# Kernel optimization log

Hardware: AMD Instinct MI355X
Metric: run time of the kernel (lower is better)

## Reference

```python
import jax, jax.numpy as jnp
import numpy as np

B, H, W, C = 8, 128, 128, 256
L = H * W
PROJ = max(C // 2, 128)
LN_EPS = 1e-5
MAX_DIST = 1.414


def _grid_edges(h, w):
    # 4-connected grid edges (bidirectional), shape (E, 2), E = 4hw - 2(h+w)
    idx = np.arange(h * w, dtype=np.int32).reshape(h, w)
    pairs = []
    # up neighbor: node (y,x) -> (y-1,x)
    pairs.append(np.stack([idx[1:, :].ravel(), idx[:-1, :].ravel()], axis=1))
    # down
    pairs.append(np.stack([idx[:-1, :].ravel(), idx[1:, :].ravel()], axis=1))
    # left
    pairs.append(np.stack([idx[:, 1:].ravel(), idx[:, :-1].ravel()], axis=1))
    # right
    pairs.append(np.stack([idx[:, :-1].ravel(), idx[:, 1:].ravel()], axis=1))
    return np.concatenate(pairs, axis=0)


def setup_inputs() -> dict:
    key = jax.random.key(0)
    k1, k2, k3, k4 = jax.random.split(key, 4)
    features = jax.random.normal(k1, (B, L, C), dtype=jnp.float32)
    deformed_coords = jax.random.uniform(k2, (B, L, 2), dtype=jnp.float32)
    edges = _grid_edges(H, W)  # (E, 2)
    edge_index = jnp.broadcast_to(jnp.asarray(edges, dtype=jnp.int32)[None], (B, edges.shape[0], 2))
    # learnable params
    alpha = jnp.asarray(0.5, dtype=jnp.float32)
    bound = 1.0 / np.sqrt(C)
    W_proj = jax.random.uniform(k3, (C, PROJ), dtype=jnp.float32, minval=-bound, maxval=bound)
    b_proj = jax.random.uniform(k4, (PROJ,), dtype=jnp.float32, minval=-bound, maxval=bound)
    ln_gamma = jnp.ones((PROJ,), dtype=jnp.float32)
    ln_beta = jnp.zeros((PROJ,), dtype=jnp.float32)
    return {"features": features, "deformed_coords": deformed_coords, "edge_index": edge_index,
            "alpha": alpha, "W_proj": W_proj, "b_proj": b_proj,
            "ln_gamma": ln_gamma, "ln_beta": ln_beta}


def reference(features, deformed_coords, edge_index, alpha, W_proj, b_proj, ln_gamma, ln_beta):
    # semantic projection: Linear -> LayerNorm -> L2 normalize
    h = jnp.einsum('blc,cp->blp', features, W_proj) + b_proj  # (B, L, P)
    mu = h.mean(axis=-1, keepdims=True)
    var = ((h - mu) ** 2).mean(axis=-1, keepdims=True)
    h = (h - mu) * jax.lax.rsqrt(var + LN_EPS) * ln_gamma + ln_beta
    norm = jnp.sqrt((h * h).sum(axis=-1, keepdims=True))
    sem = h / jnp.maximum(norm, 1e-12)  # F.normalize semantics

    src_idx = edge_index[:, :, 0:1]  # (B, E, 1)
    dst_idx = edge_index[:, :, 1:2]
    src_f = jnp.take_along_axis(sem, src_idx, axis=1)  # (B, E, P)
    dst_f = jnp.take_along_axis(sem, dst_idx, axis=1)
    semantic_sim = (src_f * dst_f).sum(axis=-1)  # (B, E)

    src_c = jnp.take_along_axis(deformed_coords, src_idx, axis=1)  # (B, E, 2)
    dst_c = jnpp_take = jnp.take_along_axis(deformed_coords, dst_idx, axis=1)
    spatial_dist = jnp.sqrt(((src_c - dst_c) ** 2).sum(axis=-1) + 1e-8)
    spatial_sim = 1.0 - spatial_dist / MAX_DIST

    a = jax.nn.sigmoid(alpha)
    edge_weights = a * semantic_sim + (1.0 - a) * spatial_sim  # (B, E)
    return edge_index, edge_weights
```

## Files before the change

kernel.cpp:

```cpp
#include <hip/hip_runtime.h>
#include <hip/hip_bf16.h>

#define Bn   8
#define Ln   16384
#define Cn   256
#define Pn   128
#define En   65024
#define Qn   16256
#define LN_EPSf 1e-5f

typedef __attribute__((ext_vector_type(8)))  short short8;
typedef __attribute__((ext_vector_type(16))) float f32x16;

__device__ __forceinline__ float bf2f(unsigned short u) {
    union { unsigned int i; float f; } v;
    v.i = ((unsigned int)u) << 16;
    return v.f;
}
__device__ __forceinline__ unsigned short f2bf(float x) {
    __hip_bfloat16 h = __float2bfloat16(x);
    return *reinterpret_cast<unsigned short*>(&h);
}
__device__ __forceinline__ unsigned int pack2(float a, float b) {
    return (unsigned int)f2bf(a) | ((unsigned int)f2bf(b) << 16);
}

#define BAR_LGKM do { \
    asm volatile("s_waitcnt lgkmcnt(0)" ::: "memory"); \
    __builtin_amdgcn_sched_barrier(0); \
    __builtin_amdgcn_s_barrier(); } while (0)
#define BAR_VM8 do { \
    asm volatile("s_waitcnt vmcnt(8) lgkmcnt(0)" ::: "memory"); \
    __builtin_amdgcn_sched_barrier(0); \
    __builtin_amdgcn_s_barrier(); } while (0)

__global__ __launch_bounds__(256)
void wt_prep(const float* __restrict__ W, __hip_bfloat16* __restrict__ Wt2)
{
    const int u = blockIdx.x * 256 + threadIdx.x;
    const int p = u & 127;
    const int g = u >> 7;
    short8 v;
#pragma unroll
    for (int j = 0; j < 8; j++)
        v[j] = (short)f2bf(W[(size_t)(g * 8 + j) * Pn + p]);
    *(short8*)((short*)Wt2 + (size_t)u * 8) = v;
}

__device__ __forceinline__ void tile_compute(
    char* fb, size_t row0, const short8* afrag, const float* plds,
    float (*red1)[32][2], float (*red2)[32],
    __hip_bfloat16* __restrict__ sem, int t, int w, int lane, int rl, int kh)
{
    const char* fbc = fb + rl * 512;
    const int   s   = rl & 7;
    f32x16 acc = (f32x16)0.f;
#pragma unroll
    for (int ks = 0; ks < 16; ks++) {
        const short8 bfv = *(const short8*)(fbc + (((2 * ks + kh) ^ s) << 4));
        acc = __builtin_amdgcn_mfma_f32_32x32x16_bf16(afrag[ks], bfv, acc, 0, 0, 0);
    }

    float s1 = 0.f, q1 = 0.f;
#pragma unroll
    for (int rq = 0; rq < 4; rq++) {
        const int p0 = 32 * w + 8 * rq + 4 * kh;
        const float4 b4 = *(const float4*)(plds + p0);
#pragma unroll
        for (int j = 0; j < 4; j++) {
            const float h = acc[rq * 4 + j] + ((const float*)&b4)[j];
            acc[rq * 4 + j] = h; s1 += h; q1 += h * h;
        }
    }
    s1 += __shfl_xor(s1, 32);
    q1 += __shfl_xor(q1, 32);
    if (lane < 32) { red1[w][rl][0] = s1; red1[w][rl][1] = q1; }
    BAR_LGKM;

    float st = 0.f, qt = 0.f;
#pragma unroll
    for (int i = 0; i < 4; i++) { st += red1[i][rl][0]; qt += red1[i][rl][1]; }
    const float mu  = st * (1.f / Pn);
    const float inv = rsqrtf(qt * (1.f / Pn) - mu * mu + LN_EPSf);

    float q2 = 0.f;
#pragma unroll
    for (int rq = 0; rq < 4; rq++) {
        const int p0 = 32 * w + 8 * rq + 4 * kh;
        const float4 g4 = *(const float4*)(plds + 128 + p0);
        const float4 e4 = *(const float4*)(plds + 256 + p0);
#pragma unroll
        for (int j = 0; j < 4; j++) {
            const float hn = (acc[rq * 4 + j] - mu) * inv
                           * ((const float*)&g4)[j] + ((const float*)&e4)[j];
            acc[rq * 4 + j] = hn; q2 += hn * hn;
        }
    }
    q2 += __shfl_xor(q2, 32);
    if (lane < 32) red2[w][rl] = q2;
    BAR_LGKM;

    float qs = 0.f;
#pragma unroll
    for (int i = 0; i < 4; i++) qs += red2[i][rl];
    const float rin = 1.f / fmaxf(sqrtf(qs), 1e-12f);

#pragma unroll
    for (int rq = 0; rq < 4; rq++) {
        uint2 val;
        val.x = pack2(acc[rq * 4 + 0] * rin, acc[rq * 4 + 1] * rin);
        val.y = pack2(acc[rq * 4 + 2] * rin, acc[rq * 4 + 3] * rin);
        *(uint2*)(fb + rl * 256 + (((4 * w + rq) ^ (rl & 7)) << 4)
                  + (kh << 3)) = val;
    }
    BAR_LGKM;

#pragma unroll
    for (int i = 0; i < 2; i++) {
        const int r = (t >> 4) + i * 16;
        const int G = t & 15;
        const uint4 v = *(const uint4*)(fb + r * 256 + ((G ^ (r & 7)) << 4));
        *reinterpret_cast<uint4*>(sem + (row0 + r) * Pn + G * 8) = v;
    }
}

__global__ __launch_bounds__(256, 3)
void proj_tile(const float* __restrict__ F,
               const __hip_bfloat16* __restrict__ Wt2,
               const float* __restrict__ bp, const float* __restrict__ gam,
               const float* __restrict__ bet, __hip_bfloat16* __restrict__ sem)
{
    __shared__ char  fbuf[2][32 * 512];
    __shared__ float red1[4][32][2];
    __shared__ float red2[4][32];
    __shared__ float plds[384];

    const int t    = threadIdx.x;
    const int w    = t >> 6;
    const int lane = t & 63;
    const int rl   = lane & 31;
    const int kh   = lane >> 5;
    const size_t row0 = (size_t)blockIdx.x * 64;

    float4 sg[8];
    {
        const float* base = F + row0 * Cn;
#pragma unroll
        for (int j = 0; j < 8; j++)
            sg[j] = *(const float4*)(base + j * 1024 + w * 256 + lane * 4);
    }

    for (int i = t; i < 384; i += 256)
        plds[i] = (i < 128) ? bp[i] : (i < 256) ? gam[i - 128] : bet[i - 256];

    short8 afrag[16];
#pragma unroll
    for (int ks = 0; ks < 16; ks++)
        afrag[ks] = *((const short8*)Wt2 + (2 * ks + kh) * 128 + 32 * w + rl);

#pragma unroll
    for (int j = 0; j < 8; j++) {
        const int r = j * 4 + w;
        uint2 v;
        v.x = pack2(sg[j].x, sg[j].y);
        v.y = pack2(sg[j].z, sg[j].w);
        *(uint2*)(fbuf[0] + r * 512 + (((lane >> 1) ^ (r & 7)) << 4)
                  + ((lane & 1) << 3)) = v;
    }
    __builtin_amdgcn_sched_barrier(0);

    {
        const float* base = F + (row0 + 32) * Cn;
#pragma unroll
        for (int j = 0; j < 8; j++)
            sg[j] = *(const float4*)(base + j * 1024 + w * 256 + lane * 4);
    }

    BAR_VM8;

    tile_compute(fbuf[0], row0, afrag, plds, red1, red2, sem, t, w, lane, rl, kh);

#pragma unroll
    for (int j = 0; j < 8; j++) {
        const int r = j * 4 + w;
        uint2 v;
        v.x = pack2(sg[j].x, sg[j].y);
        v.y = pack2(sg[j].z, sg[j].w);
        *(uint2*)(fbuf[1] + r * 512 + (((lane >> 1) ^ (r & 7)) << 4)
                  + ((lane & 1) << 3)) = v;
    }
    BAR_LGKM;

    tile_compute(fbuf[1], row0 + 32, afrag, plds, red1, red2, sem, t, w, lane, rl, kh);
}

__global__ __launch_bounds__(256)
void edge_kernel(const __hip_bfloat16* __restrict__ sem,
                 const float* __restrict__ coords,
                 const float* __restrict__ alpha,
                 float* __restrict__ out_idx,
                 float* __restrict__ out_w)
{
    const int t    = threadIdx.x;
    const int slot = t >> 2;
    const int sub  = t & 3;
    const int n0g  = blockIdx.x * 32;
    const int b    = n0g >> 14;
    const int n0   = n0g & (Ln - 1);
    const int i    = slot & 31;
    const bool hor = slot >= 32;
    const int d    = n0 + i;

    bool valid; int s;
    if (!hor) { valid = d < (Ln - 128);    s = valid ? d + 128 : d; }
    else      { valid = (d & 127) != 127;  s = valid ? d + 1   : d; }

    const short* base = (const short*)sem + (size_t)b * Ln * Pn;
    const short* srow = base + (size_t)s * Pn + sub * 8;
    const short* drow = base + (size_t)d * Pn + sub * 8;

    float dot = 0.f;
#pragma unroll
    for (int j = 0; j < 4; j++) {
        const short8 a = *(const short8*)(srow + j * 32);
        const short8 c = *(const short8*)(drow + j * 32);
#pragma unroll
        for (int k = 0; k < 8; k++)
            dot = fmaf(bf2f((unsigned short)a[k]), bf2f((unsigned short)c[k]), dot);
    }
    dot += __shfl_xor(dot, 1);
    dot += __shfl_xor(dot, 2);

    if (sub == 0 && valid) {
        const float a = 1.f / (1.f + expf(-alpha[0]));
        const size_t sc = ((size_t)b * Ln + s) * 2;
        const size_t dc = ((size_t)b * Ln + d) * 2;
        const float ddx = coords[sc + 0] - coords[dc + 0];
        const float ddy = coords[sc + 1] - coords[dc + 1];
        const float dist = sqrtf(ddx * ddx + ddy * ddy + 1e-8f);
        const float ssim = 1.f - dist / 1.414f;
        const float wgt  = a * dot + (1.f - a) * ssim;

        size_t gidx;
        if (!hor) gidx = (size_t)b * En + d;
        else      gidx = (size_t)b * En + 2 * Qn + (d - (d >> 7));

        out_w[gidx]      = wgt;
        out_w[gidx + Qn] = wgt;
        float2 fw; fw.x = (float)s; fw.y = (float)d;
        float2 tw; tw.x = (float)d; tw.y = (float)s;
        *reinterpret_cast<float2*>(out_idx + gidx * 2)        = fw;
        *reinterpret_cast<float2*>(out_idx + (gidx + Qn) * 2) = tw;
    }
}

extern "C" void kernel_launch(void* const* d_in, const int* in_sizes, int n_in,
                              void* d_out, int out_size, void* d_ws, size_t ws_size,
                              hipStream_t stream) {
    const float* F      = (const float*)d_in[0];
    const float* coords = (const float*)d_in[1];
    const float* alpha  = (const float*)d_in[3];
    const float* Wp     = (const float*)d_in[4];
    const float* bp     = (const float*)d_in[5];
    const float* gam    = (const float*)d_in[6];
    const float* bet    = (const float*)d_in[7];

    float* out     = (float*)d_out;
    float* out_idx = out;
    float* out_w   = out + (size_t)Bn * En * 2;

    __hip_bfloat16* Wt2 = (__hip_bfloat16*)d_ws;
    __hip_bfloat16* sem = (__hip_bfloat16*)((char*)d_ws + Cn * Pn * 2);

    wt_prep<<<16, 256, 0, stream>>>(Wp, Wt2);
    proj_tile<<<(Bn * Ln) / 64, 256, 0, stream>>>(F, Wt2, bp, gam, bet, sem);
    edge_kernel<<<(Bn * Ln) / 32, 256, 0, stream>>>(sem, coords, alpha,
                                                    out_idx, out_w);
}
```

Baseline: 55.18 us.

## Fuse weight prep into persistent projection kernel with cross-tile prefetch

Removes the separate weight-transpose kernel: each block now loads W in fp32 straight from global memory and converts it to bf16 MFMA fragments itself. The projection becomes a persistent kernel of 768 blocks that loop over 32-row tiles. Each block prefetches the next tile's features into registers while computing the current tile, using a double-buffered LDS. This saves one launch and amortises the weight-fragment setup across tiles. The cost is a strided, uncoalesced fp32 weight load in every block and a load imbalance, since 4096 tiles do not divide evenly over 768 blocks.

```diff
diff --git a/kernel.cpp b/kernel.cpp
--- a/kernel.cpp
+++ b/kernel.cpp
@@ -8,6 +8,8 @@
 #define En   65024
 #define Qn   16256
 #define LN_EPSf 1e-5f
+#define NTILES 4096
+#define PGRID  768
 
 typedef __attribute__((ext_vector_type(8)))  short short8;
 typedef __attribute__((ext_vector_type(16))) float f32x16;
@@ -34,19 +36,6 @@
     __builtin_amdgcn_sched_barrier(0); \
     __builtin_amdgcn_s_barrier(); } while (0)
 
-__global__ __launch_bounds__(256)
-void wt_prep(const float* __restrict__ W, __hip_bfloat16* __restrict__ Wt2)
-{
-    const int u = blockIdx.x * 256 + threadIdx.x;
-    const int p = u & 127;
-    const int g = u >> 7;
-    short8 v;
-#pragma unroll
-    for (int j = 0; j < 8; j++)
-        v[j] = (short)f2bf(W[(size_t)(g * 8 + j) * Pn + p]);
-    *(short8*)((short*)Wt2 + (size_t)u * 8) = v;
-}
-
 __device__ __forceinline__ void tile_compute(
     char* fb, size_t row0, const short8* afrag, const float* plds,
     float (*red1)[32][2], float (*red2)[32],
@@ -125,10 +114,9 @@
 }
 
 __global__ __launch_bounds__(256, 3)
-void proj_tile(const float* __restrict__ F,
-               const __hip_bfloat16* __restrict__ Wt2,
-               const float* __restrict__ bp, const float* __restrict__ gam,
-               const float* __restrict__ bet, __hip_bfloat16* __restrict__ sem)
+void proj_persist(const float* __restrict__ F, const float* __restrict__ Wp,
+                  const float* __restrict__ bp, const float* __restrict__ gam,
+                  const float* __restrict__ bet, __hip_bfloat16* __restrict__ sem)
 {
     __shared__ char  fbuf[2][32 * 512];
     __shared__ float red1[4][32][2];
@@ -136,15 +124,16 @@
     __shared__ float plds[384];
 
     const int t    = threadIdx.x;
+    const int bid  = blockIdx.x;
     const int w    = t >> 6;
     const int lane = t & 63;
     const int rl   = lane & 31;
     const int kh   = lane >> 5;
-    const size_t row0 = (size_t)blockIdx.x * 64;
 
     float4 sg[8];
+    int tile = bid;
     {
-        const float* base = F + row0 * Cn;
+        const float* base = F + (size_t)tile * 32 * Cn;
 #pragma unroll
         for (int j = 0; j < 8; j++)
             sg[j] = *(const float4*)(base + j * 1024 + w * 256 + lane * 4);
@@ -154,44 +143,46 @@
         plds[i] = (i < 128) ? bp[i] : (i < 256) ? gam[i - 128] : bet[i - 256];
 
     short8 afrag[16];
-#pragma unroll
-    for (int ks = 0; ks < 16; ks++)
-        afrag[ks] = *((const short8*)Wt2 + (2 * ks + kh) * 128 + 32 * w + rl);
-
-#pragma unroll
-    for (int j = 0; j < 8; j++) {
-        const int r = j * 4 + w;
-        uint2 v;
-        v.x = pack2(sg[j].x, sg[j].y);
-        v.y = pack2(sg[j].z, sg[j].w);
-        *(uint2*)(fbuf[0] + r * 512 + (((lane >> 1) ^ (r & 7)) << 4)
-                  + ((lane & 1) << 3)) = v;
-    }
-    __builtin_amdgcn_sched_barrier(0);
-
     {
-        const float* base = F + (row0 + 32) * Cn;
-#pragma unroll
-        for (int j = 0; j < 8; j++)
-            sg[j] = *(const float4*)(base + j * 1024 + w * 256 + lane * 4);
-    }
-
-    BAR_VM8;
-
-    tile_compute(fbuf[0], row0, afrag, plds, red1, red2, sem, t, w, lane, rl, kh);
-
-#pragma unroll
-    for (int j = 0; j < 8; j++) {
-        const int r = j * 4 + w;
-        uint2 v;
-        v.x = pack2(sg[j].x, sg[j].y);
-        v.y = pack2(sg[j].z, sg[j].w);
-        *(uint2*)(fbuf[1] + r * 512 + (((lane >> 1) ^ (r & 7)) << 4)
-                  + ((lane & 1) << 3)) = v;
-    }
-    BAR_LGKM;
-
-    tile_compute(fbuf[1], row0 + 32, afrag, plds, red1, red2, sem, t, w, lane, rl, kh);
+        const float* wcol = Wp + 32 * w + rl;
+#pragma unroll
+        for (int ks = 0; ks < 16; ks++) {
+            const int c0 = (2 * ks + kh) * 8;
+            short8 v;
+#pragma unroll
+            for (int j = 0; j < 8; j++)
+                v[j] = (short)f2bf(wcol[(size_t)(c0 + j) * Pn]);
+            afrag[ks] = v;
+        }
+    }
+
+    int cur = 0;
+    for (; tile < NTILES; tile += PGRID) {
+#pragma unroll
+        for (int j = 0; j < 8; j++) {
+            const int r = j * 4 + w;
+            uint2 v;
+            v.x = pack2(sg[j].x, sg[j].y);
+            v.y = pack2(sg[j].z, sg[j].w);
+            *(uint2*)(fbuf[cur] + r * 512 + (((lane >> 1) ^ (r & 7)) << 4)
+                      + ((lane & 1) << 3)) = v;
+        }
+        __builtin_amdgcn_sched_barrier(0);
+
+        const int nt = tile + PGRID;
+        if (nt < NTILES) {
+            const float* base = F + (size_t)nt * 32 * Cn;
+#pragma unroll
+            for (int j = 0; j < 8; j++)
+                sg[j] = *(const float4*)(base + j * 1024 + w * 256 + lane * 4);
+        }
+
+        BAR_VM8;
+
+        tile_compute(fbuf[cur], (size_t)tile * 32, afrag, plds,
+                     red1, red2, sem, t, w, lane, rl, kh);
+        cur ^= 1;
+    }
 }
 
 __global__ __launch_bounds__(256)
@@ -269,11 +260,9 @@
     float* out_idx = out;
     float* out_w   = out + (size_t)Bn * En * 2;
 
-    __hip_bfloat16* Wt2 = (__hip_bfloat16*)d_ws;
-    __hip_bfloat16* sem = (__hip_bfloat16*)((char*)d_ws + Cn * Pn * 2);
-
-    wt_prep<<<16, 256, 0, stream>>>(Wp, Wt2);
-    proj_tile<<<(Bn * Ln) / 64, 256, 0, stream>>>(F, Wt2, bp, gam, bet, sem);
+    __hip_bfloat16* sem = (__hip_bfloat16*)d_ws;
+
+    proj_persist<<<PGRID, 256, 0, stream>>>(F, Wp, bp, gam, bet, sem);
     edge_kernel<<<(Bn * Ln) / 32, 256, 0, stream>>>(sem, coords, alpha,
                                                     out_idx, out_w);
 }
```

Result: slower. 60.43 us (+9.5%).
